# Kernel optimization log

Measured on AMD Instinct MI355X. Metric: run time of the kernel, lower is better.

Reference implementation:

```python
import jax, jax.numpy as jnp
import numpy as np

S = 2048          # total tokens (single sequence)
H = 2560          # hidden size
NH = 8            # query heads
NKV = 4           # kv heads
D = 256           # head dim
EPS = 1e-6
SCALING = 256.0 ** -0.5          # query_pre_attn_scalar ** -0.5
WINDOW = 1024 - 1                # config.sliding_window - 1
ROPE_THETA = 10000.0             # rope_local_base_freq (sliding layer)


def setup_inputs() -> dict:
    key = jax.random.key(0)
    ks = jax.random.split(key, 5)
    hidden_states = jax.random.normal(ks[0], (S, H), dtype=jnp.float32)
    # RoPE tables (default rope type, HF convention: freqs duplicated along last dim)
    inv_freq = 1.0 / (ROPE_THETA ** (np.arange(0, D, 2, dtype=np.float32) / D))
    pos = np.arange(S, dtype=np.float32)
    freqs = np.outer(pos, inv_freq)                 # [S, D/2]
    emb = np.concatenate([freqs, freqs], axis=-1)   # [S, D]
    cos = jnp.asarray(np.cos(emb), dtype=jnp.float32)
    sin = jnp.asarray(np.sin(emb), dtype=jnp.float32)
    w_qkv = jax.random.normal(ks[1], (H, (NH + 2 * NKV) * D), dtype=jnp.float32) * (H ** -0.5)
    w_o = jax.random.normal(ks[2], (NH * D, H), dtype=jnp.float32) * ((NH * D) ** -0.5)
    q_norm_w = jax.random.normal(ks[3], (D,), dtype=jnp.float32) * 0.02
    k_norm_w = jax.random.normal(ks[4], (D,), dtype=jnp.float32) * 0.02
    return {"hidden_states": hidden_states, "cos": cos, "sin": sin,
            "w_qkv": w_qkv, "w_o": w_o, "q_norm_w": q_norm_w, "k_norm_w": k_norm_w}


def _rms_norm(x, w):
    # Gemma3RMSNorm: x * rsqrt(mean(x^2)+eps) * (1 + w), computed in fp32
    var = jnp.mean(jnp.square(x), axis=-1, keepdims=True)
    return x * jax.lax.rsqrt(var + EPS) * (1.0 + w)


def _rotate_half(x):
    x1, x2 = jnp.split(x, 2, axis=-1)
    return jnp.concatenate([-x2, x1], axis=-1)


def reference(hidden_states, cos, sin, w_qkv, w_o, q_norm_w, k_norm_w):
    qkv = hidden_states @ w_qkv                          # [S, (NH+2NKV)*D]
    q, k, v = jnp.split(qkv, [NH * D, (NH + NKV) * D], axis=-1)
    q = q.reshape(S, NH, D)
    k = k.reshape(S, NKV, D)
    v = v.reshape(S, NKV, D)

    # per-head QK RMSNorm
    q = _rms_norm(q, q_norm_w)
    k = _rms_norm(k, k_norm_w)

    # RoPE (cos/sin broadcast over heads)
    c = cos[:, None, :]
    s = sin[:, None, :]
    q = q * c + _rotate_half(q) * s
    k = k * c + _rotate_half(k) * s

    # GQA expand kv heads
    rep = NH // NKV
    k = jnp.repeat(k, rep, axis=1)                       # [S, NH, D]
    v = jnp.repeat(v, rep, axis=1)

    scores = jnp.einsum('snd,tnd->nst', q, k) * SCALING  # [NH, S, S]
    i = jnp.arange(S)[:, None]
    j = jnp.arange(S)[None, :]
    allowed = (j <= i) & (i - j <= WINDOW)               # causal sliding window
    scores = jnp.where(allowed[None], scores, jnp.finfo(scores.dtype).min)
    probs = jax.nn.softmax(scores, axis=-1)
    attn = jnp.einsum('nst,tnd->snd', probs, v)          # [S, NH, D]
    out = attn.reshape(S, NH * D) @ w_o                  # [S, H]
    return out
```

## Files before the change

### kernel.cpp

```cpp
#include <hip/hip_runtime.h>
#include <hip/hip_bf16.h>
#include <cstdint>
#include <cstddef>

#define S_LEN 2048
#define HID   2560
#define NHQ   8
#define QKV_N 4096
#define ATT_N 2048
#define WIN   1023
#define SCALE 0.0625f
#define NINF  -3.0e38f

typedef __attribute__((ext_vector_type(8))) short bf16x8;
typedef __attribute__((ext_vector_type(4))) float f32x4;

__device__ __forceinline__ unsigned bf_hi(float f) {
  unsigned u = __builtin_bit_cast(unsigned, f);
  return (u + 0x7FFFu + ((u >> 16) & 1u)) >> 16;
}
__device__ __forceinline__ float bf_to_f(unsigned h) {
  return __builtin_bit_cast(float, h << 16);
}
__device__ __forceinline__ void g2l16(const void* g, void* l) {
  __builtin_amdgcn_global_load_lds((const __attribute__((address_space(1))) void*)g,
                                   (__attribute__((address_space(3))) void*)l,
                                   16, 0, 0);
}

__global__ __launch_bounds__(256) void split_transpose(const float* __restrict__ W,
                                                       unsigned short* __restrict__ Th,
                                                       unsigned short* __restrict__ Tl,
                                                       int K, int N) {
  __shared__ float tile[32][33];
  const int tid = threadIdx.x;
  const int kt = blockIdx.y * 32, nt = blockIdx.x * 32;
  {
    const int r = tid >> 3, c = (tid & 7) * 4;
    const float4 v = *(const float4*)(W + (size_t)(kt + r) * N + nt + c);
    tile[r][c] = v.x; tile[r][c + 1] = v.y; tile[r][c + 2] = v.z; tile[r][c + 3] = v.w;
  }
  __syncthreads();
  const int nl = tid >> 3, k = (tid & 7) * 4;
  unsigned hw[2], lw[2];
  #pragma unroll
  for (int j = 0; j < 2; ++j) {
    const float f0 = tile[k + 2 * j][nl], f1 = tile[k + 2 * j + 1][nl];
    const unsigned h0 = bf_hi(f0), h1 = bf_hi(f1);
    const float r0 = f0 - bf_to_f(h0), r1 = f1 - bf_to_f(h1);
    hw[j] = h0 | (h1 << 16);
    lw[j] = bf_hi(r0) | (bf_hi(r1) << 16);
  }
  *(uint2*)(Th + (size_t)(nt + nl) * K + kt + k) = make_uint2(hw[0], hw[1]);
  *(uint2*)(Tl + (size_t)(nt + nl) * K + kt + k) = make_uint2(lw[0], lw[1]);
}

__global__ __launch_bounds__(256) void gemm_split(const float* __restrict__ A,
                                                  const unsigned short* __restrict__ BTh,
                                                  const unsigned short* __restrict__ BTl,
                                                  float* __restrict__ C,
                                                  int M, int N, int K, int nbx) {
  __shared__ __align__(16) unsigned short As_h[128][40];
  __shared__ __align__(16) unsigned short As_l[128][40];
  __shared__ __align__(16) unsigned short Bs_h[128][40];
  __shared__ __align__(16) unsigned short Bs_l[128][40];

  const int tid = threadIdx.x;
  int bid = blockIdx.x;
  const int cpx = gridDim.x >> 3;
  bid = (bid & 7) * cpx + (bid >> 3);
  const int bm = (bid / nbx) * 128;
  const int bn = (bid % nbx) * 128;

  const int lane = tid & 63;
  const int wv = tid >> 6;
  const int wr = (wv >> 1) * 64;
  const int wc = (wv & 1) * 64;
  const int frow = lane & 15;
  const int kl = (lane >> 4) * 8;

  const int srow = tid >> 1;
  const int sseg = (tid & 1) * 16;

  f32x4 acc[4][4] = {};

  const float* aptr = A + (size_t)(bm + srow) * K + sseg;
  const unsigned short* bhp = BTh + (size_t)(bn + srow) * K + sseg;
  const unsigned short* blp = BTl + (size_t)(bn + srow) * K + sseg;

  for (int k0 = 0; k0 < K; k0 += 32) {
    float4 fa[4];
    #pragma unroll
    for (int j = 0; j < 4; ++j) fa[j] = *(const float4*)(aptr + k0 + j * 4);
    const uint4 bh0 = *(const uint4*)(bhp + k0);
    const uint4 bh1 = *(const uint4*)(bhp + k0 + 8);
    const uint4 bl0 = *(const uint4*)(blp + k0);
    const uint4 bl1 = *(const uint4*)(blp + k0 + 8);

    __syncthreads();

    unsigned hw[8], lw[8];
    #pragma unroll
    for (int j = 0; j < 4; ++j) {
      const float f[4] = {fa[j].x, fa[j].y, fa[j].z, fa[j].w};
      #pragma unroll
      for (int p = 0; p < 2; ++p) {
        const float f0 = f[2 * p], f1 = f[2 * p + 1];
        const unsigned h0 = bf_hi(f0), h1 = bf_hi(f1);
        const float r0 = f0 - bf_to_f(h0), r1 = f1 - bf_to_f(h1);
        hw[j * 2 + p] = h0 | (h1 << 16);
        lw[j * 2 + p] = bf_hi(r0) | (bf_hi(r1) << 16);
      }
    }
    *(uint4*)&As_h[srow][sseg]     = make_uint4(hw[0], hw[1], hw[2], hw[3]);
    *(uint4*)&As_h[srow][sseg + 8] = make_uint4(hw[4], hw[5], hw[6], hw[7]);
    *(uint4*)&As_l[srow][sseg]     = make_uint4(lw[0], lw[1], lw[2], lw[3]);
    *(uint4*)&As_l[srow][sseg + 8] = make_uint4(lw[4], lw[5], lw[6], lw[7]);
    *(uint4*)&Bs_h[srow][sseg]     = bh0;
    *(uint4*)&Bs_h[srow][sseg + 8] = bh1;
    *(uint4*)&Bs_l[srow][sseg]     = bl0;
    *(uint4*)&Bs_l[srow][sseg + 8] = bl1;
    __syncthreads();

    bf16x8 ah[4], al[4], bhf[4], blf[4];
    #pragma unroll
    for (int i = 0; i < 4; ++i) {
      ah[i]  = *(const bf16x8*)&As_h[wr + i * 16 + frow][kl];
      al[i]  = *(const bf16x8*)&As_l[wr + i * 16 + frow][kl];
      bhf[i] = *(const bf16x8*)&Bs_h[wc + i * 16 + frow][kl];
      blf[i] = *(const bf16x8*)&Bs_l[wc + i * 16 + frow][kl];
    }
    #pragma unroll
    for (int i = 0; i < 4; ++i)
      #pragma unroll
      for (int j = 0; j < 4; ++j) {
        acc[i][j] = __builtin_amdgcn_mfma_f32_16x16x32_bf16(ah[i], bhf[j], acc[i][j], 0, 0, 0);
        acc[i][j] = __builtin_amdgcn_mfma_f32_16x16x32_bf16(ah[i], blf[j], acc[i][j], 0, 0, 0);
        acc[i][j] = __builtin_amdgcn_mfma_f32_16x16x32_bf16(al[i], bhf[j], acc[i][j], 0, 0, 0);
      }
  }

  #pragma unroll
  for (int i = 0; i < 4; ++i) {
    const int r0 = bm + wr + i * 16 + (lane >> 4) * 4;
    #pragma unroll
    for (int j = 0; j < 4; ++j) {
      const int c = bn + wc + j * 16 + frow;
      #pragma unroll
      for (int r = 0; r < 4; ++r)
        C[(size_t)(r0 + r) * N + c] = acc[i][j][r];
    }
  }
}

__global__ __launch_bounds__(256) void qk_norm_rope_split(
    const float* __restrict__ qkv, const float* __restrict__ cosp,
    const float* __restrict__ sinp, const float* __restrict__ qw,
    const float* __restrict__ kw,
    unsigned short* __restrict__ Qh, unsigned short* __restrict__ Ql,
    unsigned short* __restrict__ Kh, unsigned short* __restrict__ Kl) {
  const int lane = threadIdx.x & 63;
  const int wave = threadIdx.x >> 6;
  const int row  = blockIdx.x * 4 + wave;
  const int s    = row / 12;
  const int c    = row % 12;
  const float* p = qkv + (size_t)s * QKV_N + c * 256;

  float4 x = *(const float4*)(p + lane * 4);
  float ss = x.x * x.x + x.y * x.y + x.z * x.z + x.w * x.w;
  #pragma unroll
  for (int off = 32; off; off >>= 1) ss += __shfl_xor(ss, off);
  const float scale = rsqrtf(ss * (1.0f / 256.0f) + 1e-6f);

  const float* wp = (c < 8) ? qw : kw;
  float4 w4 = *(const float4*)(wp + lane * 4);
  float y0 = x.x * scale * (1.0f + w4.x);
  float y1 = x.y * scale * (1.0f + w4.y);
  float y2 = x.z * scale * (1.0f + w4.z);
  float y3 = x.w * scale * (1.0f + w4.w);

  float z0 = __shfl_xor(y0, 32);
  float z1 = __shfl_xor(y1, 32);
  float z2 = __shfl_xor(y2, 32);
  float z3 = __shfl_xor(y3, 32);
  const float sgn = (lane < 32) ? -1.0f : 1.0f;

  float4 c4 = *(const float4*)(cosp + (size_t)s * 256 + lane * 4);
  float4 s4 = *(const float4*)(sinp + (size_t)s * 256 + lane * 4);
  float o[4];
  o[0] = y0 * c4.x + sgn * z0 * s4.x;
  o[1] = y1 * c4.y + sgn * z1 * s4.y;
  o[2] = y2 * c4.z + sgn * z2 * s4.z;
  o[3] = y3 * c4.w + sgn * z3 * s4.w;

  const float mul = (c < 8) ? SCALE : 1.0f;
  #pragma unroll
  for (int j = 0; j < 4; ++j) o[j] *= mul;

  unsigned h[4], lo[4];
  #pragma unroll
  for (int j = 0; j < 4; ++j) {
    h[j] = bf_hi(o[j]);
    lo[j] = bf_hi(o[j] - bf_to_f(h[j]));
  }
  const size_t off = ((c < 8) ? ((size_t)c * S_LEN + s)
                              : ((size_t)(c - 8) * S_LEN + s)) * 256 + lane * 4;
  unsigned short* dh = (c < 8 ? Qh : Kh) + off;
  unsigned short* dl = (c < 8 ? Ql : Kl) + off;
  *(uint2*)dh = make_uint2(h[0] | (h[1] << 16), h[2] | (h[3] << 16));
  *(uint2*)dl = make_uint2(lo[0] | (lo[1] << 16), lo[2] | (lo[3] << 16));
}

__global__ __launch_bounds__(256) void v_split_transpose(
    const float* __restrict__ qkv,
    unsigned short* __restrict__ VTh, unsigned short* __restrict__ VTl) {
  __shared__ float tile[32][33];
  const int tid = threadIdx.x;
  const int s0 = blockIdx.x * 32, d0 = blockIdx.y * 32, kvh = blockIdx.z;
  {
    const int r = tid >> 3, c = (tid & 7) * 4;
    const float4 v = *(const float4*)(qkv + (size_t)(s0 + r) * QKV_N + 3072 + kvh * 256 + d0 + c);
    tile[r][c] = v.x; tile[r][c + 1] = v.y; tile[r][c + 2] = v.z; tile[r][c + 3] = v.w;
  }
  __syncthreads();
  const int dd = tid >> 3, sc = (tid & 7) * 4;
  unsigned h[4], lo[4];
  #pragma unroll
  for (int j = 0; j < 4; ++j) {
    const float f = tile[sc + j][dd];
    h[j] = bf_hi(f);
    lo[j] = bf_hi(f - bf_to_f(h[j]));
  }
  const size_t off = ((size_t)kvh * 256 + d0 + dd) * S_LEN + s0 + sc;
  *(uint2*)(VTh + off) = make_uint2(h[0] | (h[1] << 16), h[2] | (h[3] << 16));
  *(uint2*)(VTl + off) = make_uint2(lo[0] | (lo[1] << 16), lo[2] | (lo[3] << 16));
}

#define KH_U  0
#define KL_U  8192
#define VTH_U 16384
#define VTL_U 24576
#define PH_U  32768
#define PL_U  34048
__global__ __launch_bounds__(128, 2) void attn_mfma(
    const unsigned short* __restrict__ Qh, const unsigned short* __restrict__ Ql,
    const unsigned short* __restrict__ Kh, const unsigned short* __restrict__ Kl,
    const unsigned short* __restrict__ VTh, const unsigned short* __restrict__ VTl,
    float* __restrict__ attn_out) {
  __shared__ __align__(16) unsigned short smem[35328];

  const int tid  = threadIdx.x;
  const int lane = tid & 63;
  const int wv   = __builtin_amdgcn_readfirstlane(tid >> 6);
  const int head = blockIdx.y;
  const int kvh  = head >> 1;
  const int q0   = blockIdx.x * 32;
  const int g16  = lane >> 4;
  const int c16  = lane & 15;

  const int qrow = q0 + wv * 16 + c16;
  bf16x8 qh[8], ql[8];
  {
    const unsigned short* qph = Qh + ((size_t)head * S_LEN + qrow) * 256 + g16 * 8;
    const unsigned short* qpl = Ql + ((size_t)head * S_LEN + qrow) * 256 + g16 * 8;
    #pragma unroll
    for (int dc = 0; dc < 8; ++dc) {
      qh[dc] = *(const bf16x8*)(qph + dc * 32);
      ql[dc] = *(const bf16x8*)(qpl + dc * 32);
    }
  }

  f32x4 o_acc[16] = {};
  float m_run[4], l_run[4];
  #pragma unroll
  for (int r = 0; r < 4; ++r) { m_run[r] = NINF; l_run[r] = 0.0f; }

  const int rmin = q0 + wv * 16, rmax = rmin + 15;
  const unsigned short* kh_g  = Kh  + (size_t)kvh * S_LEN * 256;
  const unsigned short* kl_g  = Kl  + (size_t)kvh * S_LEN * 256;
  const unsigned short* vth_g = VTh + (size_t)kvh * 256 * S_LEN;
  const unsigned short* vtl_g = VTl + (size_t)kvh * 256 * S_LEN;

  const int kstart = (q0 > WIN) ? ((q0 - WIN) & ~31) : 0;
  const int kend   = q0 + 31;

  for (int t0 = kstart; t0 <= kend; t0 += 32) {
    {
      char* lbase = (char*)smem + ((tid & ~63) << 4);
      #pragma unroll
      for (int i = 0; i < 8; ++i) {
        const int uu = i * 128 + tid, row = uu >> 5, sl = uu & 31;
        g2l16(kh_g + (size_t)(t0 + row) * 256 + ((sl ^ (row & 7)) * 8),
              lbase + i * 2048);
      }
      #pragma unroll
      for (int i = 0; i < 8; ++i) {
        const int uu = i * 128 + tid, row = uu >> 5, sl = uu & 31;
        g2l16(kl_g + (size_t)(t0 + row) * 256 + ((sl ^ (row & 7)) * 8),
              lbase + 16384 + i * 2048);
      }
      #pragma unroll
      for (int i = 0; i < 8; ++i) {
        const int uu = i * 128 + tid, d = uu >> 2, sl = uu & 3;
        g2l16(vth_g + (size_t)d * S_LEN + t0 + ((sl ^ ((d >> 1) & 3)) * 8),
              lbase + 32768 + i * 2048);
      }
      #pragma unroll
      for (int i = 0; i < 8; ++i) {
        const int uu = i * 128 + tid, d = uu >> 2, sl = uu & 3;
        g2l16(vtl_g + (size_t)d * S_LEN + t0 + ((sl ^ ((d >> 1) & 3)) * 8),
              lbase + 49152 + i * 2048);
      }
    }
    __syncthreads();

    const bool active = (t0 <= rmax) && (t0 + 31 + WIN >= rmin);
    if (active) {
      f32x4 sa[2] = {};
      #pragma unroll
      for (int t = 0; t < 2; ++t) {
        const int krow = t * 16 + c16;
        const int swz = krow & 7;
        #pragma unroll
        for (int dc = 0; dc < 8; ++dc) {
          const int sl = ((dc * 4 + g16) ^ swz) * 16;
          const bf16x8 kfh = *(const bf16x8*)((const char*)smem + krow * 512 + sl);
          const bf16x8 kfl = *(const bf16x8*)((const char*)smem + 16384 + krow * 512 + sl);
          sa[t] = __builtin_amdgcn_mfma_f32_16x16x32_bf16(qh[dc], kfh, sa[t], 0, 0, 0);
          sa[t] = __builtin_amdgcn_mfma_f32_16x16x32_bf16(qh[dc], kfl, sa[t], 0, 0, 0);
          sa[t] = __builtin_amdgcn_mfma_f32_16x16x32_bf16(ql[dc], kfh, sa[t], 0, 0, 0);
        }
      }

      const int k0c = t0 + c16;
      #pragma unroll
      for (int r = 0; r < 4; ++r) {
        const int q = rmin + g16 * 4 + r;
        const bool v0 = (k0c <= q) && (q - k0c <= WIN);
        const bool v1 = (k0c + 16 <= q) && (q - (k0c + 16) <= WIN);
        float s0 = v0 ? sa[0][r] : NINF;
        float s1 = v1 ? sa[1][r] : NINF;
        float mx = fmaxf(s0, s1);
        #pragma unroll
        for (int off = 8; off; off >>= 1) mx = fmaxf(mx, __shfl_xor(mx, off));
        const float m_new = fmaxf(m_run[r], mx);
        const float rs = __expf(m_run[r] - m_new);
        const float p0 = v0 ? __expf(s0 - m_new) : 0.0f;
        const float p1 = v1 ? __expf(s1 - m_new) : 0.0f;
        float psum = p0 + p1;
        #pragma unroll
        for (int off = 8; off; off >>= 1) psum += __shfl_xor(psum, off);
        l_run[r] = l_run[r] * rs + psum;
        m_run[r] = m_new;
        #pragma unroll
        for (int dt = 0; dt < 16; ++dt) o_acc[dt][r] *= rs;
        const int pro = wv * 640 + (g16 * 4 + r) * 40;
        const unsigned h0 = bf_hi(p0), h1 = bf_hi(p1);
        smem[PH_U + pro + c16]      = (unsigned short)h0;
        smem[PH_U + pro + 16 + c16] = (unsigned short)h1;
        smem[PL_U + pro + c16]      = (unsigned short)bf_hi(p0 - bf_to_f(h0));
        smem[PL_U + pro + 16 + c16] = (unsigned short)bf_hi(p1 - bf_to_f(h1));
      }

      const bf16x8 pah = *(const bf16x8*)&smem[PH_U + wv * 640 + c16 * 40 + g16 * 8];
      const bf16x8 pal = *(const bf16x8*)&smem[PL_U + wv * 640 + c16 * 40 + g16 * 8];
      #pragma unroll
      for (int dt = 0; dt < 16; ++dt) {
        const int vrow = dt * 16 + c16;
        const int sl = (g16 ^ ((vrow >> 1) & 3)) * 16;
        const bf16x8 vfh = *(const bf16x8*)((const char*)smem + 32768 + vrow * 64 + sl);
        const bf16x8 vfl = *(const bf16x8*)((const char*)smem + 49152 + vrow * 64 + sl);
        o_acc[dt] = __builtin_amdgcn_mfma_f32_16x16x32_bf16(pah, vfh, o_acc[dt], 0, 0, 0);
        o_acc[dt] = __builtin_amdgcn_mfma_f32_16x16x32_bf16(pah, vfl, o_acc[dt], 0, 0, 0);
        o_acc[dt] = __builtin_amdgcn_mfma_f32_16x16x32_bf16(pal, vfh, o_acc[dt], 0, 0, 0);
      }
    }
    __syncthreads();
  }

  #pragma unroll
  for (int r = 0; r < 4; ++r) {
    const float inv = 1.0f / l_run[r];
    float* orow = attn_out + (size_t)(rmin + g16 * 4 + r) * ATT_N + head * 256 + c16;
    #pragma unroll
    for (int dt = 0; dt < 16; ++dt) orow[dt * 16] = o_acc[dt][r] * inv;
  }
}

extern "C" void kernel_launch(void* const* d_in, const int* in_sizes, int n_in,
                              void* d_out, int out_size, void* d_ws, size_t ws_size,
                              hipStream_t stream) {
  const float* hs    = (const float*)d_in[0];
  const float* cosp  = (const float*)d_in[1];
  const float* sinp  = (const float*)d_in[2];
  const float* w_qkv = (const float*)d_in[3];
  const float* w_o   = (const float*)d_in[4];
  const float* qw    = (const float*)d_in[5];
  const float* kw    = (const float*)d_in[6];
  float* out = (float*)d_out;

  const size_t MB = 1024 * 1024;
  char* ws = (char*)d_ws;
  float* qkv = (float*)ws;
  unsigned short* wh = (unsigned short*)(ws + 32 * MB);
  unsigned short* wl = (unsigned short*)(ws + 52 * MB);
  unsigned short* Qh = (unsigned short*)(ws + 32 * MB);
  unsigned short* Ql = (unsigned short*)(ws + 40 * MB);
  unsigned short* Kh = (unsigned short*)(ws + 48 * MB);
  unsigned short* Kl = (unsigned short*)(ws + 52 * MB);
  unsigned short* VTh = (unsigned short*)(ws + 56 * MB);
  unsigned short* VTl = (unsigned short*)(ws + 60 * MB);
  float* attn = (float*)ws;
  unsigned short* oh = (unsigned short*)(ws + 16 * MB);
  unsigned short* ol = (unsigned short*)(ws + 26 * MB);

  split_transpose<<<dim3(QKV_N / 32, HID / 32), 256, 0, stream>>>(
      w_qkv, wh, wl, HID, QKV_N);
  gemm_split<<<(S_LEN / 128) * (QKV_N / 128), 256, 0, stream>>>(
      hs, wh, wl, qkv, S_LEN, QKV_N, HID, QKV_N / 128);
  qk_norm_rope_split<<<(S_LEN * 12) / 4, 256, 0, stream>>>(
      qkv, cosp, sinp, qw, kw, Qh, Ql, Kh, Kl);
  v_split_transpose<<<dim3(S_LEN / 32, 256 / 32, 4), 256, 0, stream>>>(
      qkv, VTh, VTl);
  attn_mfma<<<dim3(S_LEN / 32, NHQ), 128, 0, stream>>>(
      Qh, Ql, Kh, Kl, VTh, VTl, attn);
  split_transpose<<<dim3(HID / 32, ATT_N / 32), 256, 0, stream>>>(
      w_o, oh, ol, ATT_N, HID);
  gemm_split<<<(S_LEN / 128) * (HID / 128), 256, 0, stream>>>(
      attn, oh, ol, out, S_LEN, HID, ATT_N, HID / 128);
}
```

Baseline: 569.2 us.

## Pre-split GEMM A operands to bf16 and load tiles via direct global-to-LDS

The hidden states are split into bf16 hi/lo halves by a separate kernel (stored temporarily in the output buffer), and attention now writes its output directly as bf16 hi/lo pairs. This lets the GEMM kernel drop its per-tile fp32 conversion and stage all four operands with async global_load_lds into a swizzled LDS layout. The attention grid is remapped so that blocks sharing a kv head land on the same XCD for L2 reuse. The cost is an extra split pass plus reuse of d_out as scratch, which is safe only because the final GEMM reads its A operand from other buffers.

```diff
diff --git a/kernel.cpp b/kernel.cpp
--- a/kernel.cpp
+++ b/kernel.cpp
@@ -26,6 +26,25 @@
   __builtin_amdgcn_global_load_lds((const __attribute__((address_space(1))) void*)g,
                                    (__attribute__((address_space(3))) void*)l,
                                    16, 0, 0);
+}
+
+__global__ __launch_bounds__(256) void split_rows(const float* __restrict__ X,
+                                                  unsigned short* __restrict__ Xh,
+                                                  unsigned short* __restrict__ Xl) {
+  const size_t i = ((size_t)blockIdx.x * 256 + threadIdx.x) * 8;
+  const float4 v0 = *(const float4*)(X + i);
+  const float4 v1 = *(const float4*)(X + i + 4);
+  const float f[8] = {v0.x, v0.y, v0.z, v0.w, v1.x, v1.y, v1.z, v1.w};
+  unsigned hw[4], lw[4];
+  #pragma unroll
+  for (int j = 0; j < 4; ++j) {
+    const unsigned h0 = bf_hi(f[2 * j]), h1 = bf_hi(f[2 * j + 1]);
+    const float r0 = f[2 * j] - bf_to_f(h0), r1 = f[2 * j + 1] - bf_to_f(h1);
+    hw[j] = h0 | (h1 << 16);
+    lw[j] = bf_hi(r0) | (bf_hi(r1) << 16);
+  }
+  *(uint4*)(Xh + i) = make_uint4(hw[0], hw[1], hw[2], hw[3]);
+  *(uint4*)(Xl + i) = make_uint4(lw[0], lw[1], lw[2], lw[3]);
 }
 
 __global__ __launch_bounds__(256) void split_transpose(const float* __restrict__ W,
@@ -55,15 +74,11 @@
   *(uint2*)(Tl + (size_t)(nt + nl) * K + kt + k) = make_uint2(lw[0], lw[1]);
 }
 
-__global__ __launch_bounds__(256) void gemm_split(const float* __restrict__ A,
-                                                  const unsigned short* __restrict__ BTh,
-                                                  const unsigned short* __restrict__ BTl,
-                                                  float* __restrict__ C,
-                                                  int M, int N, int K, int nbx) {
-  __shared__ __align__(16) unsigned short As_h[128][40];
-  __shared__ __align__(16) unsigned short As_l[128][40];
-  __shared__ __align__(16) unsigned short Bs_h[128][40];
-  __shared__ __align__(16) unsigned short Bs_l[128][40];
+__global__ __launch_bounds__(256) void gemm_bf16_split(
+    const unsigned short* __restrict__ Ah, const unsigned short* __restrict__ Al,
+    const unsigned short* __restrict__ Bh, const unsigned short* __restrict__ Bl,
+    float* __restrict__ C, int M, int N, int K, int nbx) {
+  __shared__ __align__(16) unsigned short smem[16384];
 
   const int tid = threadIdx.x;
   int bid = blockIdx.x;
@@ -77,78 +92,67 @@
   const int wr = (wv >> 1) * 64;
   const int wc = (wv & 1) * 64;
   const int frow = lane & 15;
-  const int kl = (lane >> 4) * 8;
-
-  const int srow = tid >> 1;
-  const int sseg = (tid & 1) * 16;
+  const int g16 = lane >> 4;
+
+  const int u0 = tid, u1 = tid + 256;
+  const int r0 = u0 >> 2, s0 = (u0 & 3) ^ ((r0 >> 1) & 3);
+  const int r1 = u1 >> 2, s1 = (u1 & 3) ^ ((r1 >> 1) & 3);
+
+  const unsigned short* a_h = Ah + (size_t)bm * K;
+  const unsigned short* a_l = Al + (size_t)bm * K;
+  const unsigned short* b_h = Bh + (size_t)bn * K;
+  const unsigned short* b_l = Bl + (size_t)bn * K;
+
+  unsigned short* d0 = smem + ((tid & ~63) << 3);
+  unsigned short* d1 = smem + 2048 + ((tid & ~63) << 3);
+
+  const int sx = (g16 ^ ((frow >> 1) & 3)) * 8;
 
   f32x4 acc[4][4] = {};
 
-  const float* aptr = A + (size_t)(bm + srow) * K + sseg;
-  const unsigned short* bhp = BTh + (size_t)(bn + srow) * K + sseg;
-  const unsigned short* blp = BTl + (size_t)(bn + srow) * K + sseg;
-
   for (int k0 = 0; k0 < K; k0 += 32) {
-    float4 fa[4];
-    #pragma unroll
-    for (int j = 0; j < 4; ++j) fa[j] = *(const float4*)(aptr + k0 + j * 4);
-    const uint4 bh0 = *(const uint4*)(bhp + k0);
-    const uint4 bh1 = *(const uint4*)(bhp + k0 + 8);
-    const uint4 bl0 = *(const uint4*)(blp + k0);
-    const uint4 bl1 = *(const uint4*)(blp + k0 + 8);
-
     __syncthreads();
-
-    unsigned hw[8], lw[8];
-    #pragma unroll
-    for (int j = 0; j < 4; ++j) {
-      const float f[4] = {fa[j].x, fa[j].y, fa[j].z, fa[j].w};
-      #pragma unroll
-      for (int p = 0; p < 2; ++p) {
-        const float f0 = f[2 * p], f1 = f[2 * p + 1];
-        const unsigned h0 = bf_hi(f0), h1 = bf_hi(f1);
-        const float r0 = f0 - bf_to_f(h0), r1 = f1 - bf_to_f(h1);
-        hw[j * 2 + p] = h0 | (h1 << 16);
-        lw[j * 2 + p] = bf_hi(r0) | (bf_hi(r1) << 16);
-      }
-    }
-    *(uint4*)&As_h[srow][sseg]     = make_uint4(hw[0], hw[1], hw[2], hw[3]);
-    *(uint4*)&As_h[srow][sseg + 8] = make_uint4(hw[4], hw[5], hw[6], hw[7]);
-    *(uint4*)&As_l[srow][sseg]     = make_uint4(lw[0], lw[1], lw[2], lw[3]);
-    *(uint4*)&As_l[srow][sseg + 8] = make_uint4(lw[4], lw[5], lw[6], lw[7]);
-    *(uint4*)&Bs_h[srow][sseg]     = bh0;
-    *(uint4*)&Bs_h[srow][sseg + 8] = bh1;
-    *(uint4*)&Bs_l[srow][sseg]     = bl0;
-    *(uint4*)&Bs_l[srow][sseg + 8] = bl1;
+    {
+      const size_t o0 = (size_t)r0 * K + k0 + s0 * 8;
+      const size_t o1 = (size_t)r1 * K + k0 + s1 * 8;
+      g2l16(a_h + o0, d0);
+      g2l16(a_h + o1, d1);
+      g2l16(a_l + o0, d0 + 4096);
+      g2l16(a_l + o1, d1 + 4096);
+      g2l16(b_h + o0, d0 + 8192);
+      g2l16(b_h + o1, d1 + 8192);
+      g2l16(b_l + o0, d0 + 12288);
+      g2l16(b_l + o1, d1 + 12288);
+    }
     __syncthreads();
 
-    bf16x8 ah[4], al[4], bhf[4], blf[4];
+    bf16x8 ah[4], al[4], bh[4], bl[4];
     #pragma unroll
     for (int i = 0; i < 4; ++i) {
-      ah[i]  = *(const bf16x8*)&As_h[wr + i * 16 + frow][kl];
-      al[i]  = *(const bf16x8*)&As_l[wr + i * 16 + frow][kl];
-      bhf[i] = *(const bf16x8*)&Bs_h[wc + i * 16 + frow][kl];
-      blf[i] = *(const bf16x8*)&Bs_l[wc + i * 16 + frow][kl];
+      ah[i] = *(const bf16x8*)&smem[(wr + i * 16 + frow) * 32 + sx];
+      al[i] = *(const bf16x8*)&smem[4096 + (wr + i * 16 + frow) * 32 + sx];
+      bh[i] = *(const bf16x8*)&smem[8192 + (wc + i * 16 + frow) * 32 + sx];
+      bl[i] = *(const bf16x8*)&smem[12288 + (wc + i * 16 + frow) * 32 + sx];
     }
     #pragma unroll
     for (int i = 0; i < 4; ++i)
       #pragma unroll
       for (int j = 0; j < 4; ++j) {
-        acc[i][j] = __builtin_amdgcn_mfma_f32_16x16x32_bf16(ah[i], bhf[j], acc[i][j], 0, 0, 0);
-        acc[i][j] = __builtin_amdgcn_mfma_f32_16x16x32_bf16(ah[i], blf[j], acc[i][j], 0, 0, 0);
-        acc[i][j] = __builtin_amdgcn_mfma_f32_16x16x32_bf16(al[i], bhf[j], acc[i][j], 0, 0, 0);
+        acc[i][j] = __builtin_amdgcn_mfma_f32_16x16x32_bf16(ah[i], bh[j], acc[i][j], 0, 0, 0);
+        acc[i][j] = __builtin_amdgcn_mfma_f32_16x16x32_bf16(ah[i], bl[j], acc[i][j], 0, 0, 0);
+        acc[i][j] = __builtin_amdgcn_mfma_f32_16x16x32_bf16(al[i], bh[j], acc[i][j], 0, 0, 0);
       }
   }
 
   #pragma unroll
   for (int i = 0; i < 4; ++i) {
-    const int r0 = bm + wr + i * 16 + (lane >> 4) * 4;
+    const int row0 = bm + wr + i * 16 + g16 * 4;
     #pragma unroll
     for (int j = 0; j < 4; ++j) {
       const int c = bn + wc + j * 16 + frow;
       #pragma unroll
       for (int r = 0; r < 4; ++r)
-        C[(size_t)(r0 + r) * N + c] = acc[i][j][r];
+        C[(size_t)(row0 + r) * N + c] = acc[i][j][r];
     }
   }
 }
@@ -236,25 +240,23 @@
   *(uint2*)(VTl + off) = make_uint2(lo[0] | (lo[1] << 16), lo[2] | (lo[3] << 16));
 }
 
-#define KH_U  0
-#define KL_U  8192
-#define VTH_U 16384
-#define VTL_U 24576
 #define PH_U  32768
 #define PL_U  34048
 __global__ __launch_bounds__(128, 2) void attn_mfma(
     const unsigned short* __restrict__ Qh, const unsigned short* __restrict__ Ql,
     const unsigned short* __restrict__ Kh, const unsigned short* __restrict__ Kl,
     const unsigned short* __restrict__ VTh, const unsigned short* __restrict__ VTl,
-    float* __restrict__ attn_out) {
+    unsigned short* __restrict__ Oh, unsigned short* __restrict__ Ol) {
   __shared__ __align__(16) unsigned short smem[35328];
 
   const int tid  = threadIdx.x;
   const int lane = tid & 63;
   const int wv   = __builtin_amdgcn_readfirstlane(tid >> 6);
-  const int head = blockIdx.y;
-  const int kvh  = head >> 1;
-  const int q0   = blockIdx.x * 32;
+  const int b    = blockIdx.x;
+  const int xcd  = b & 7;
+  const int kvh  = xcd >> 1;
+  const int head = kvh * 2 + ((b >> 3) & 1);
+  const int q0   = (((b >> 4) << 1) | (xcd & 1)) * 32;
   const int g16  = lane >> 4;
   const int c16  = lane & 15;
 
@@ -381,9 +383,14 @@
   #pragma unroll
   for (int r = 0; r < 4; ++r) {
     const float inv = 1.0f / l_run[r];
-    float* orow = attn_out + (size_t)(rmin + g16 * 4 + r) * ATT_N + head * 256 + c16;
+    const size_t rowo = (size_t)(rmin + g16 * 4 + r) * ATT_N + head * 256 + c16;
     #pragma unroll
-    for (int dt = 0; dt < 16; ++dt) orow[dt * 16] = o_acc[dt][r] * inv;
+    for (int dt = 0; dt < 16; ++dt) {
+      const float o = o_acc[dt][r] * inv;
+      const unsigned h = bf_hi(o);
+      Oh[rowo + dt * 16] = (unsigned short)h;
+      Ol[rowo + dt * 16] = (unsigned short)bf_hi(o - bf_to_f(h));
+    }
   }
 }
 
@@ -397,7 +404,6 @@
   const float* w_o   = (const float*)d_in[4];
   const float* qw    = (const float*)d_in[5];
   const float* kw    = (const float*)d_in[6];
-  float* out = (float*)d_out;
 
   const size_t MB = 1024 * 1024;
   char* ws = (char*)d_ws;
@@ -410,22 +416,26 @@
   unsigned short* Kl = (unsigned short*)(ws + 52 * MB);
   unsigned short* VTh = (unsigned short*)(ws + 56 * MB);
   unsigned short* VTl = (unsigned short*)(ws + 60 * MB);
-  float* attn = (float*)ws;
+  unsigned short* Oh = (unsigned short*)ws;
+  unsigned short* Ol = (unsigned short*)(ws + 8 * MB);
   unsigned short* oh = (unsigned short*)(ws + 16 * MB);
   unsigned short* ol = (unsigned short*)(ws + 26 * MB);
-
+  unsigned short* Ahs = (unsigned short*)d_out;
+  unsigned short* Als = Ahs + (size_t)S_LEN * HID;
+  float* out = (float*)d_out;
+
+  split_rows<<<(S_LEN * HID) / (256 * 8), 256, 0, stream>>>(hs, Ahs, Als);
   split_transpose<<<dim3(QKV_N / 32, HID / 32), 256, 0, stream>>>(
       w_qkv, wh, wl, HID, QKV_N);
-  gemm_split<<<(S_LEN / 128) * (QKV_N / 128), 256, 0, stream>>>(
-      hs, wh, wl, qkv, S_LEN, QKV_N, HID, QKV_N / 128);
+  gemm_bf16_split<<<(S_LEN / 128) * (QKV_N / 128), 256, 0, stream>>>(
+      Ahs, Als, wh, wl, qkv, S_LEN, QKV_N, HID, QKV_N / 128);
   qk_norm_rope_split<<<(S_LEN * 12) / 4, 256, 0, stream>>>(
       qkv, cosp, sinp, qw, kw, Qh, Ql, Kh, Kl);
   v_split_transpose<<<dim3(S_LEN / 32, 256 / 32, 4), 256, 0, stream>>>(
       qkv, VTh, VTl);
-  attn_mfma<<<dim3(S_LEN / 32, NHQ), 128, 0, stream>>>(
-      Qh, Ql, Kh, Kl, VTh, VTl, attn);
+  attn_mfma<<<512, 128, 0, stream>>>(Qh, Ql, Kh, Kl, VTh, VTl, Oh, Ol);
   split_transpose<<<dim3(HID / 32, ATT_N / 32), 256, 0, stream>>>(
       w_o, oh, ol, ATT_N, HID);
-  gemm_split<<<(S_LEN / 128) * (HID / 128), 256, 0, stream>>>(
-      attn, oh, ol, out, S_LEN, HID, ATT_N, HID / 128);
-}
+  gemm_bf16_split<<<(S_LEN / 128) * (HID / 128), 256, 0, stream>>>(
+      Oh, Ol, oh, ol, out, S_LEN, HID, ATT_N, HID / 128);
+}
```

New measurement: 502.4 us. 1.13x faster.
